# Performance work log

Hardware: AMD Instinct MI355X
Metric: run time of the kernel (lower is better)

The kernel has to match this reference:

```python
import jax, jax.numpy as jnp
import numpy as np

N, E = 100000, 1000000
IN_F, HID, OUT, K = 64, 64, 32, 3


def setup_inputs() -> dict:
    key = jax.random.key(0)
    ks = jax.random.split(key, 8)
    s = 0.05
    return {
        "features": jax.random.normal(ks[0], (N, IN_F), dtype=jnp.float32),
        "src": jax.random.randint(ks[1], (E,), 0, N),
        "dst": jax.random.randint(ks[2], (E,), 0, N),
        "n_nodes": N,
        "W1": jax.random.normal(ks[3], (K * IN_F, HID), jnp.float32) * s,
        "b1": jnp.zeros((HID,), jnp.float32),
        "W2": jax.random.normal(ks[4], (K * HID, HID), jnp.float32) * s,
        "b2": jnp.zeros((HID,), jnp.float32),
        "Wm1": jax.random.normal(ks[5], (HID, HID), jnp.float32) * s,
        "bm1": jnp.zeros((HID,), jnp.float32),
        "Wm2": jax.random.normal(ks[6], (HID, OUT), jnp.float32) * s,
        "bm2": jnp.zeros((OUT,), jnp.float32),
    }


def _cheb_conv(x, src, dst, dinv, W, b, n_nodes, k=K):
    # DGL ChebConv with lambda_max = 2 (re_norm = 2/lambda_max = 1).
    def prop(h):  # D^{-1/2} A D^{-1/2} h via edge gather/scatter
        m = (h * dinv)[src]                                   # [E, F]
        agg = jax.ops.segment_sum(m, dst, num_segments=n_nodes)
        return agg * dinv

    X0 = x
    Xs = [X0]
    X1 = -prop(X0)                 # -re_norm*L h + (re_norm-1)*X0, re_norm=1
    Xs.append(X1)
    for _ in range(2, k):
        Xi = -2.0 * prop(X1) - X0  # Chebyshev recursion
        Xs.append(Xi)
        X0, X1 = X1, Xi
    return jnp.concatenate(Xs, axis=1) @ W + b  # Linear(k*F_in -> F_out)


def reference(features, src, dst, n_nodes, W1, b1, W2, b2, Wm1, bm1, Wm2, bm2):
    deg = jax.ops.segment_sum(
        jnp.ones((src.shape[0],), dtype=features.dtype), dst, num_segments=n_nodes
    )
    dinv = (jnp.clip(deg, 1.0, None) ** -0.5)[:, None]  # in-degree^{-1/2}
    x = jax.nn.relu(_cheb_conv(features, src, dst, dinv, W1, b1, n_nodes))
    x = jax.nn.relu(_cheb_conv(x, src, dst, dinv, W2, b2, n_nodes))
    return jax.nn.relu(x @ Wm1 + bm1) @ Wm2 + bm2
```

## Files before the change

kernel.cpp:

```cpp
#include <hip/hip_runtime.h>


typedef unsigned short ushort_t;
typedef __attribute__((ext_vector_type(8))) short v8s;
typedef __attribute__((ext_vector_type(4))) float v4f;

__device__ inline ushort_t f2bf(float f) {
    unsigned u = __float_as_uint(f);
    return (ushort_t)((u + 0x7FFFu + ((u >> 16) & 1u)) >> 16);
}
__device__ inline float bf2f(ushort_t h) {
    return __uint_as_float(((unsigned)h) << 16);
}

#define BSH 9
#define BSZ (1 << BSH)
#define CHUNK 4096

__global__ void k_wprep(const float* __restrict__ W1, const float* __restrict__ W2,
                        const float* __restrict__ Wm1, const float* __restrict__ Wm2,
                        ushort_t* __restrict__ W1t, ushort_t* __restrict__ W2t,
                        ushort_t* __restrict__ Wm1t, ushort_t* __restrict__ Wm2t,
                        int* __restrict__ gbase, int NB) {
    int i = blockIdx.x * 256 + threadIdx.x;
    if (i < 12288) { int k = i >> 6, n = i & 63; W1t[n * 192 + k] = f2bf(W1[i]); return; }
    i -= 12288;
    if (i < 12288) { int k = i >> 6, n = i & 63; W2t[n * 192 + k] = f2bf(W2[i]); return; }
    i -= 12288;
    if (i < 4096) { int k = i >> 6, n = i & 63; Wm1t[n * 64 + k] = f2bf(Wm1[i]); return; }
    i -= 4096;
    if (i < 2048) { int k = i >> 5, n = i & 31; Wm2t[n * 64 + k] = f2bf(Wm2[i]); return; }
    i -= 2048;
    if (i < NB) gbase[i] = 0;
}


__global__ __launch_bounds__(256) void k_bhist(const int* __restrict__ dst,
                                               int* __restrict__ gbase, int E, int NB) {
    __shared__ int h[1024];
    for (int i = threadIdx.x; i < NB; i += 256) h[i] = 0;
    __syncthreads();
    for (int i = blockIdx.x * blockDim.x + threadIdx.x; i < E; i += gridDim.x * blockDim.x)
        atomicAdd(&h[dst[i] >> BSH], 1);
    __syncthreads();
    for (int i = threadIdx.x; i < NB; i += 256)
        if (h[i]) atomicAdd(&gbase[i], h[i]);
}

__global__ void k_bscan(int* __restrict__ gbase, int* __restrict__ gcur, int NB) {
    __shared__ int sh[1024];
    int t = threadIdx.x;
    int v = (t < NB) ? gbase[t] : 0;
    sh[t] = v;
    __syncthreads();
    for (int off = 1; off < 1024; off <<= 1) {
        int u = 0;
        if (t >= off) u = sh[t - off];
        __syncthreads();
        sh[t] += u;
        __syncthreads();
    }
    if (t < NB) {
        int excl = sh[t] - v;
        gbase[t] = excl;
        gcur[t] = excl;
    }
}

__global__ __launch_bounds__(256) void k_bucket2(
    const int* __restrict__ src, const int* __restrict__ dst,
    int* __restrict__ gcur, int2* __restrict__ eb, int E, int NB) {
    __shared__ int ls[CHUNK];
    __shared__ int ld[CHUNK];
    __shared__ int hist[1024];
    __shared__ int bbase[1024];
    int t = threadIdx.x;
    int base = blockIdx.x * CHUNK;
    int count = E - base;
    if (count > CHUNK) count = CHUNK;
    for (int i = t; i < NB; i += 256) hist[i] = 0;
    __syncthreads();
    for (int i = t; i < count; i += 256) {
        int s = src[base + i];
        int d = dst[base + i];
        ls[i] = s;
        ld[i] = d;
        atomicAdd(&hist[d >> BSH], 1);
    }
    __syncthreads();
    for (int b = t; b < NB; b += 256) {
        int c = hist[b];
        bbase[b] = c ? atomicAdd(&gcur[b], c) : 0;
        hist[b] = 0;
    }
    __syncthreads();
    for (int i = t; i < count; i += 256) {
        int d = ld[i];
        int b = d >> BSH;
        int off = atomicAdd(&hist[b], 1);
        eb[bbase[b] + off] = make_int2(ls[i], d);
    }
}

__global__ __launch_bounds__(256) void k_local(
    const int2* __restrict__ eb, const int* __restrict__ gbase,
    int* __restrict__ col, int* __restrict__ row_ptr,
    float* __restrict__ dinv, int N, int E, int NB) {
    __shared__ int cnt[BSZ];
    __shared__ int tsum[256];
    int t = threadIdx.x;
    int b = blockIdx.x;
    int d0 = b << BSH;
    cnt[2 * t] = 0;
    cnt[2 * t + 1] = 0;
    __syncthreads();
    int beg = gbase[b];
    int end = (b + 1 < NB) ? gbase[b + 1] : E;
    for (int i = beg + t; i < end; i += 256)
        atomicAdd(&cnt[eb[i].y - d0], 1);
    __syncthreads();
    int c0 = cnt[2 * t], c1 = cnt[2 * t + 1];
    int mysum = c0 + c1;
    tsum[t] = mysum;
    __syncthreads();
    for (int off = 1; off < 256; off <<= 1) {
        int u = 0;
        if (t >= off) u = tsum[t - off];
        __syncthreads();
        tsum[t] += u;
        __syncthreads();
    }
    int rbase = beg + tsum[t] - mysum;
    int d = d0 + 2 * t;
    if (d < N) {
        row_ptr[d] = rbase;
        dinv[d] = rsqrtf(fmaxf((float)c0, 1.0f));
    }
    if (d + 1 < N) {
        row_ptr[d + 1] = rbase + c0;
        dinv[d + 1] = rsqrtf(fmaxf((float)c1, 1.0f));
    }
    cnt[2 * t] = rbase;
    cnt[2 * t + 1] = rbase + c0;
    __syncthreads();
    for (int i = beg + t; i < end; i += 256) {
        int2 e = eb[i];
        int p = atomicAdd(&cnt[e.y - d0], 1);
        col[p] = e.x;
    }
    if (b == NB - 1 && t == 0) row_ptr[N] = E;
}

__global__ void k_tobf16(const float4* __restrict__ X, const float* __restrict__ dinv,
                         ushort4* __restrict__ Y, int n4) {
    int i = blockIdx.x * blockDim.x + threadIdx.x;
    if (i < n4) {
        float s = dinv[i >> 4];
        float4 v = X[i];
        ushort4 o;
        o.x = f2bf(v.x * s); o.y = f2bf(v.y * s); o.z = f2bf(v.z * s); o.w = f2bf(v.w * s);
        Y[i] = o;
    }
}

template <int MODE>
__global__ __launch_bounds__(256) void k_prop(
    const ushort_t* __restrict__ Xb, const int* __restrict__ rp,
    const int* __restrict__ col, const float* __restrict__ dinv,
    const ushort_t* __restrict__ X0b, ushort_t* __restrict__ OUTB, int N) {
    int wid = (blockIdx.x * blockDim.x + threadIdx.x) >> 6;
    int lane = threadIdx.x & 63;
    if (wid >= N) return;
    int g = lane >> 4;
    int fl = (lane & 15) * 4;
    int beg = rp[wid], end = rp[wid + 1];
    float4 a0 = make_float4(0.f, 0.f, 0.f, 0.f);
    float4 a1 = make_float4(0.f, 0.f, 0.f, 0.f);
    int e = beg + g;
    for (; e + 4 < end; e += 8) {
        int s0 = col[e], s1 = col[e + 4];
        ushort4 u0 = *(const ushort4*)&Xb[(size_t)s0 * 64 + fl];
        ushort4 u1 = *(const ushort4*)&Xb[(size_t)s1 * 64 + fl];
        a0.x += bf2f(u0.x); a0.y += bf2f(u0.y); a0.z += bf2f(u0.z); a0.w += bf2f(u0.w);
        a1.x += bf2f(u1.x); a1.y += bf2f(u1.y); a1.z += bf2f(u1.z); a1.w += bf2f(u1.w);
    }
    if (e < end) {
        int s0 = col[e];
        ushort4 u0 = *(const ushort4*)&Xb[(size_t)s0 * 64 + fl];
        a0.x += bf2f(u0.x); a0.y += bf2f(u0.y); a0.z += bf2f(u0.z); a0.w += bf2f(u0.w);
    }
    float4 acc;
    acc.x = a0.x + a1.x;
    acc.y = a0.y + a1.y;
    acc.z = a0.z + a1.z;
    acc.w = a0.w + a1.w;
    acc.x += __shfl_xor(acc.x, 16);
    acc.y += __shfl_xor(acc.y, 16);
    acc.z += __shfl_xor(acc.z, 16);
    acc.w += __shfl_xor(acc.w, 16);
    acc.x += __shfl_xor(acc.x, 32);
    acc.y += __shfl_xor(acc.y, 32);
    acc.z += __shfl_xor(acc.z, 32);
    acc.w += __shfl_xor(acc.w, 32);
    if (g == 0) {
        float di = dinv[wid];
        ushort4 ob;
        if (MODE == 1) {
            float m = -di * di;
            ob.x = f2bf(m * acc.x);
            ob.y = f2bf(m * acc.y);
            ob.z = f2bf(m * acc.z);
            ob.w = f2bf(m * acc.w);
        } else {
            ushort4 x0u = *(const ushort4*)&X0b[(size_t)wid * 64 + fl];
            float m = -2.0f * di;
            float rd = 1.0f / di;
            ob.x = f2bf(fmaf(m, acc.x, -rd * bf2f(x0u.x)));
            ob.y = f2bf(fmaf(m, acc.y, -rd * bf2f(x0u.y)));
            ob.z = f2bf(fmaf(m, acc.z, -rd * bf2f(x0u.z)));
            ob.w = f2bf(fmaf(m, acc.w, -rd * bf2f(x0u.w)));
        }
        *(ushort4*)&OUTB[(size_t)wid * 64 + fl] = ob;
    }
}

template <bool SCALE_OUT>
__global__ __launch_bounds__(256) void k_cheb_mfma(
    const ushort_t* __restrict__ X0, const ushort_t* __restrict__ X1,
    const ushort_t* __restrict__ X2, const float* __restrict__ dinv,
    const ushort_t* __restrict__ Wt, const float* __restrict__ b,
    ushort_t* __restrict__ Yb, int N) {
    int wave = threadIdx.x >> 6, lane = threadIdx.x & 63;
    int n16 = lane & 15, q = lane >> 4;
    int node0 = blockIdx.x * 64;
    int arow = node0 + wave * 16 + n16;
    const ushort_t* Xc[3] = {X0, X1, X2};

    v4f acc_s[4], acc_u[4];
#pragma unroll
    for (int t = 0; t < 4; t++) {
        acc_s[t] = (v4f){0.f, 0.f, 0.f, 0.f};
        acc_u[t] = (v4f){0.f, 0.f, 0.f, 0.f};
    }
#pragma unroll
    for (int ks = 0; ks < 6; ks++) {
        int c = ks >> 1;
        int kk = (ks & 1) * 32 + q * 8;
        v8s av = {0, 0, 0, 0, 0, 0, 0, 0};
        if (arow < N) av = *(const v8s*)&Xc[c][(size_t)arow * 64 + kk];
#pragma unroll
        for (int t = 0; t < 4; t++) {
            v8s bv = *(const v8s*)&Wt[(size_t)(t * 16 + n16) * 192 + ks * 32 + q * 8];
            if (c < 2)
                acc_s[t] = __builtin_amdgcn_mfma_f32_16x16x32_bf16(av, bv, acc_s[t], 0, 0, 0);
            else
                acc_u[t] = __builtin_amdgcn_mfma_f32_16x16x32_bf16(av, bv, acc_u[t], 0, 0, 0);
        }
    }
    int rbase = node0 + wave * 16 + q * 4;
#pragma unroll
    for (int r = 0; r < 4; r++) {
        int row = rbase + r;
        if (row < N) {
            float dv = dinv[row];
            float rd = 1.0f / dv;
            float s = SCALE_OUT ? dv : 1.0f;
#pragma unroll
            for (int t = 0; t < 4; t++) {
                float y = fmaf(rd, acc_s[t][r], acc_u[t][r]) + b[t * 16 + n16];
                y = fmaxf(y, 0.0f);
                Yb[(size_t)row * 64 + t * 16 + n16] = f2bf(s * y);
            }
        }
    }
}

__global__ __launch_bounds__(256) void k_mlp_mfma(
    const ushort_t* __restrict__ Hb, const ushort_t* __restrict__ W1t,
    const float* __restrict__ b1, const ushort_t* __restrict__ W2t,
    const float* __restrict__ b2, float* __restrict__ out, int N) {
    __shared__ ushort_t Hs[64][76];
    int wave = threadIdx.x >> 6, lane = threadIdx.x & 63;
    int n16 = lane & 15, q = lane >> 4;
    int node0 = blockIdx.x * 64;
    int arow = node0 + wave * 16 + n16;

    v4f acc[4];
#pragma unroll
    for (int t = 0; t < 4; t++) acc[t] = (v4f){0.f, 0.f, 0.f, 0.f};
#pragma unroll
    for (int ks = 0; ks < 2; ks++) {
        v8s av = {0, 0, 0, 0, 0, 0, 0, 0};
        if (arow < N) av = *(const v8s*)&Hb[(size_t)arow * 64 + ks * 32 + q * 8];
#pragma unroll
        for (int t = 0; t < 4; t++) {
            v8s bv = *(const v8s*)&W1t[(size_t)(t * 16 + n16) * 64 + ks * 32 + q * 8];
            acc[t] = __builtin_amdgcn_mfma_f32_16x16x32_bf16(av, bv, acc[t], 0, 0, 0);
        }
    }
    int lr = wave * 16 + q * 4;
#pragma unroll
    for (int r = 0; r < 4; r++)
#pragma unroll
        for (int t = 0; t < 4; t++) {
            float y = acc[t][r] + b1[t * 16 + n16];
            Hs[lr + r][t * 16 + n16] = f2bf(fmaxf(y, 0.0f));
        }
    __syncthreads();

    v4f a2[2];
    a2[0] = (v4f){0.f, 0.f, 0.f, 0.f};
    a2[1] = (v4f){0.f, 0.f, 0.f, 0.f};
#pragma unroll
    for (int ks = 0; ks < 2; ks++) {
        v8s av = *(const v8s*)&Hs[wave * 16 + n16][ks * 32 + q * 8];
#pragma unroll
        for (int t = 0; t < 2; t++) {
            v8s bv = *(const v8s*)&W2t[(size_t)(t * 16 + n16) * 64 + ks * 32 + q * 8];
            a2[t] = __builtin_amdgcn_mfma_f32_16x16x32_bf16(av, bv, a2[t], 0, 0, 0);
        }
    }
    int rbase = node0 + wave * 16 + q * 4;
#pragma unroll
    for (int r = 0; r < 4; r++) {
        int row = rbase + r;
        if (row < N) {
#pragma unroll
            for (int t = 0; t < 2; t++)
                out[(size_t)row * 32 + t * 16 + n16] = a2[t][r] + b2[t * 16 + n16];
        }
    }
}

extern "C" void kernel_launch(void* const* d_in, const int* in_sizes, int n_in,
                              void* d_out, int out_size, void* d_ws, size_t ws_size,
                              hipStream_t stream) {
    const float* features = (const float*)d_in[0];
    const int* src = (const int*)d_in[1];
    const int* dst = (const int*)d_in[2];
    const float* W1 = (const float*)d_in[4];
    const float* b1 = (const float*)d_in[5];
    const float* W2 = (const float*)d_in[6];
    const float* b2 = (const float*)d_in[7];
    const float* Wm1 = (const float*)d_in[8];
    const float* bm1 = (const float*)d_in[9];
    const float* Wm2 = (const float*)d_in[10];
    const float* bm2 = (const float*)d_in[11];
    float* out = (float*)d_out;

    int N = in_sizes[0] / 64;
    int E = in_sizes[1];
    int NB = (N + BSZ - 1) >> BSH;

    float* ws = (float*)d_ws;
    float* dinv = ws;
    int* row_ptr = (int*)(dinv + N);
    int* gbase = row_ptr + (N + 1);
    int* gcur = gbase + 1024;
    int* col = gcur + 1024;
    int2* eb = (int2*)(((uintptr_t)(col + E) + 7) & ~(uintptr_t)7);
    ushort_t* Fb  = (ushort_t*)(eb + E);
    ushort_t* X1b = Fb  + (size_t)N * 64;
    ushort_t* X2b = X1b + (size_t)N * 64;
    ushort_t* H1b = X2b + (size_t)N * 64;
    ushort_t* H2b = H1b + (size_t)N * 64;
    ushort_t* W1t = H2b + (size_t)N * 64;
    ushort_t* W2t = W1t + 64 * 192;
    ushort_t* Wm1t = W2t + 64 * 192;
    ushort_t* Wm2t = Wm1t + 64 * 64;

    int pblk = (N * 64 + 255) / 256;
    int gblk = (N + 63) / 64;
    int n4 = N * 16;
    int cblk = (n4 + 255) / 256;
    int bblk = (E + CHUNK - 1) / CHUNK;

    k_wprep<<<(30720 + 1024 + 255) / 256, 256, 0, stream>>>(
        W1, W2, Wm1, Wm2, W1t, W2t, Wm1t, Wm2t, gbase, NB);

    k_bhist<<<512, 256, 0, stream>>>(dst, gbase, E, NB);
    k_bscan<<<1, 1024, 0, stream>>>(gbase, gcur, NB);
    k_bucket2<<<bblk, 256, 0, stream>>>(src, dst, gcur, eb, E, NB);
    k_local<<<NB, 256, 0, stream>>>(eb, gbase, col, row_ptr, dinv, N, E, NB);

    k_tobf16<<<cblk, 256, 0, stream>>>((const float4*)features, dinv, (ushort4*)Fb, n4);

    k_prop<1><<<pblk, 256, 0, stream>>>(Fb, row_ptr, col, dinv, nullptr, X1b, N);
    k_prop<2><<<pblk, 256, 0, stream>>>(X1b, row_ptr, col, dinv, Fb, X2b, N);
    k_cheb_mfma<true><<<gblk, 256, 0, stream>>>(Fb, X1b, X2b, dinv, W1t, b1, H1b, N);

    k_prop<1><<<pblk, 256, 0, stream>>>(H1b, row_ptr, col, dinv, nullptr, X1b, N);
    k_prop<2><<<pblk, 256, 0, stream>>>(X1b, row_ptr, col, dinv, H1b, X2b, N);
    k_cheb_mfma<false><<<gblk, 256, 0, stream>>>(H1b, X1b, X2b, dinv, W2t, b2, H2b, N);

    k_mlp_mfma<<<gblk, 256, 0, stream>>>(H2b, Wm1t, bm1, Wm2t, bm2, out, N);
}
```

Before: 388.6 us.

## Build CSR with global atomic counting sort and fuse second ChebConv with MLP

Replaces the two-level bucketed CSR build (bucket histogram, bucket scatter, per-bucket local sort) with per-node global atomic degree counting, a two-pass block scan, and a direct atomic scatter into col. It also fuses the second Chebyshev linear layer with the two-layer MLP head, keeping the hidden activations in shared memory instead of writing and rereading H2. The simpler CSR build drops the intermediate edge buffer and launches, but relies on contended global atomics with random access, and column order within a row becomes nondeterministic.

Result: slower. 452.8 us (+16.5%).

```diff
diff --git a/kernel.cpp b/kernel.cpp
--- a/kernel.cpp
+++ b/kernel.cpp
@@ -12,16 +12,12 @@
 __device__ inline float bf2f(ushort_t h) {
     return __uint_as_float(((unsigned)h) << 16);
 }
-
-#define BSH 9
-#define BSZ (1 << BSH)
-#define CHUNK 4096
 
 __global__ void k_wprep(const float* __restrict__ W1, const float* __restrict__ W2,
                         const float* __restrict__ Wm1, const float* __restrict__ Wm2,
                         ushort_t* __restrict__ W1t, ushort_t* __restrict__ W2t,
                         ushort_t* __restrict__ Wm1t, ushort_t* __restrict__ Wm2t,
-                        int* __restrict__ gbase, int NB) {
+                        int* __restrict__ deg, int N) {
     int i = blockIdx.x * 256 + threadIdx.x;
     if (i < 12288) { int k = i >> 6, n = i & 63; W1t[n * 192 + k] = f2bf(W1[i]); return; }
     i -= 12288;
@@ -31,124 +27,86 @@
     i -= 4096;
     if (i < 2048) { int k = i >> 5, n = i & 31; Wm2t[n * 64 + k] = f2bf(Wm2[i]); return; }
     i -= 2048;
-    if (i < NB) gbase[i] = 0;
-}
-
-
-__global__ __launch_bounds__(256) void k_bhist(const int* __restrict__ dst,
-                                               int* __restrict__ gbase, int E, int NB) {
-    __shared__ int h[1024];
-    for (int i = threadIdx.x; i < NB; i += 256) h[i] = 0;
-    __syncthreads();
-    for (int i = blockIdx.x * blockDim.x + threadIdx.x; i < E; i += gridDim.x * blockDim.x)
-        atomicAdd(&h[dst[i] >> BSH], 1);
-    __syncthreads();
-    for (int i = threadIdx.x; i < NB; i += 256)
-        if (h[i]) atomicAdd(&gbase[i], h[i]);
-}
-
-__global__ void k_bscan(int* __restrict__ gbase, int* __restrict__ gcur, int NB) {
+    if (i < N) deg[i] = 0;
+}
+
+
+__global__ __launch_bounds__(256) void k_deg(const int* __restrict__ dst,
+                                             int* __restrict__ deg, int E) {
+    int base = blockIdx.x * 1024 + threadIdx.x;
+#pragma unroll
+    for (int k = 0; k < 4; k++) {
+        int i = base + k * 256;
+        if (i < E) atomicAdd(&deg[dst[i]], 1);
+    }
+}
+
+__global__ __launch_bounds__(1024) void k_scanA(const int* __restrict__ deg,
+                                                int* __restrict__ row_ptr,
+                                                int* __restrict__ psum,
+                                                float* __restrict__ dinv, int N) {
     __shared__ int sh[1024];
     int t = threadIdx.x;
-    int v = (t < NB) ? gbase[t] : 0;
+    int i = blockIdx.x * 1024 + t;
+    int v = (i < N) ? deg[i] : 0;
     sh[t] = v;
+    if (i < N) dinv[i] = rsqrtf(fmaxf((float)v, 1.0f));
     __syncthreads();
     for (int off = 1; off < 1024; off <<= 1) {
-        int u = 0;
-        if (t >= off) u = sh[t - off];
+        int u = (t >= off) ? sh[t - off] : 0;
         __syncthreads();
         sh[t] += u;
         __syncthreads();
     }
-    if (t < NB) {
-        int excl = sh[t] - v;
-        gbase[t] = excl;
-        gcur[t] = excl;
-    }
-}
-
-__global__ __launch_bounds__(256) void k_bucket2(
-    const int* __restrict__ src, const int* __restrict__ dst,
-    int* __restrict__ gcur, int2* __restrict__ eb, int E, int NB) {
-    __shared__ int ls[CHUNK];
-    __shared__ int ld[CHUNK];
-    __shared__ int hist[1024];
-    __shared__ int bbase[1024];
-    int t = threadIdx.x;
-    int base = blockIdx.x * CHUNK;
-    int count = E - base;
-    if (count > CHUNK) count = CHUNK;
-    for (int i = t; i < NB; i += 256) hist[i] = 0;
-    __syncthreads();
-    for (int i = t; i < count; i += 256) {
-        int s = src[base + i];
-        int d = dst[base + i];
-        ls[i] = s;
-        ld[i] = d;
-        atomicAdd(&hist[d >> BSH], 1);
-    }
-    __syncthreads();
-    for (int b = t; b < NB; b += 256) {
-        int c = hist[b];
-        bbase[b] = c ? atomicAdd(&gcur[b], c) : 0;
-        hist[b] = 0;
-    }
-    __syncthreads();
-    for (int i = t; i < count; i += 256) {
-        int d = ld[i];
-        int b = d >> BSH;
-        int off = atomicAdd(&hist[b], 1);
-        eb[bbase[b] + off] = make_int2(ls[i], d);
-    }
-}
-
-__global__ __launch_bounds__(256) void k_local(
-    const int2* __restrict__ eb, const int* __restrict__ gbase,
-    int* __restrict__ col, int* __restrict__ row_ptr,
-    float* __restrict__ dinv, int N, int E, int NB) {
-    __shared__ int cnt[BSZ];
-    __shared__ int tsum[256];
-    int t = threadIdx.x;
-    int b = blockIdx.x;
-    int d0 = b << BSH;
-    cnt[2 * t] = 0;
-    cnt[2 * t + 1] = 0;
-    __syncthreads();
-    int beg = gbase[b];
-    int end = (b + 1 < NB) ? gbase[b + 1] : E;
-    for (int i = beg + t; i < end; i += 256)
-        atomicAdd(&cnt[eb[i].y - d0], 1);
-    __syncthreads();
-    int c0 = cnt[2 * t], c1 = cnt[2 * t + 1];
-    int mysum = c0 + c1;
-    tsum[t] = mysum;
-    __syncthreads();
-    for (int off = 1; off < 256; off <<= 1) {
-        int u = 0;
-        if (t >= off) u = tsum[t - off];
-        __syncthreads();
-        tsum[t] += u;
-        __syncthreads();
-    }
-    int rbase = beg + tsum[t] - mysum;
-    int d = d0 + 2 * t;
-    if (d < N) {
-        row_ptr[d] = rbase;
-        dinv[d] = rsqrtf(fmaxf((float)c0, 1.0f));
-    }
-    if (d + 1 < N) {
-        row_ptr[d + 1] = rbase + c0;
-        dinv[d + 1] = rsqrtf(fmaxf((float)c1, 1.0f));
-    }
-    cnt[2 * t] = rbase;
-    cnt[2 * t + 1] = rbase + c0;
-    __syncthreads();
-    for (int i = beg + t; i < end; i += 256) {
-        int2 e = eb[i];
-        int p = atomicAdd(&cnt[e.y - d0], 1);
-        col[p] = e.x;
-    }
-    if (b == NB - 1 && t == 0) row_ptr[N] = E;
+    if (i < N) row_ptr[i] = sh[t] - v;
+    if (t == 1023) psum[blockIdx.x] = sh[1023];
+}
+
+__global__ __launch_bounds__(1024) void k_scanC(int* __restrict__ row_ptr,
+                                                int* __restrict__ gcur,
+                                                const int* __restrict__ psum,
+                                                int N, int E, int NBLK) {
+    __shared__ int red[17];
+    int t = threadIdx.x, b = blockIdx.x;
+    int v = (t < b) ? psum[t] : 0;
+    v += __shfl_down(v, 32);
+    v += __shfl_down(v, 16);
+    v += __shfl_down(v, 8);
+    v += __shfl_down(v, 4);
+    v += __shfl_down(v, 2);
+    v += __shfl_down(v, 1);
+    if ((t & 63) == 0) red[t >> 6] = v;
+    __syncthreads();
+    if (t == 0) {
+        int s = 0;
+        for (int w = 0; w < 16; w++) s += red[w];
+        red[16] = s;
+    }
+    __syncthreads();
+    int base = red[16];
+    int i = b * 1024 + t;
+    if (i < N) {
+        int r = row_ptr[i] + base;
+        row_ptr[i] = r;
+        gcur[i] = r;
+    }
+    if (b == NBLK - 1 && t == 0) row_ptr[N] = E;
+}
+
+__global__ __launch_bounds__(256) void k_scatter(const int* __restrict__ src,
+                                                 const int* __restrict__ dst,
+                                                 int* __restrict__ gcur,
+                                                 int* __restrict__ col, int E) {
+    int base = blockIdx.x * 1024 + threadIdx.x;
+#pragma unroll
+    for (int k = 0; k < 4; k++) {
+        int i = base + k * 256;
+        if (i < E) {
+            int s = src[i], d = dst[i];
+            int p = atomicAdd(&gcur[d], 1);
+            col[p] = s;
+        }
+    }
 }
 
 __global__ void k_tobf16(const float4* __restrict__ X, const float* __restrict__ dinv,
@@ -275,36 +233,80 @@
     }
 }
 
-__global__ __launch_bounds__(256) void k_mlp_mfma(
-    const ushort_t* __restrict__ Hb, const ushort_t* __restrict__ W1t,
-    const float* __restrict__ b1, const ushort_t* __restrict__ W2t,
-    const float* __restrict__ b2, float* __restrict__ out, int N) {
-    __shared__ ushort_t Hs[64][76];
+__global__ __launch_bounds__(256) void k_cheb_mlp(
+    const ushort_t* __restrict__ X0, const ushort_t* __restrict__ X1,
+    const ushort_t* __restrict__ X2, const float* __restrict__ dinv,
+    const ushort_t* __restrict__ Wt, const float* __restrict__ b,
+    const ushort_t* __restrict__ Wm1t, const float* __restrict__ bm1,
+    const ushort_t* __restrict__ Wm2t, const float* __restrict__ bm2,
+    float* __restrict__ out, int N) {
+    __shared__ ushort_t Hs0[64][76];
+    __shared__ ushort_t Hs1[64][76];
     int wave = threadIdx.x >> 6, lane = threadIdx.x & 63;
     int n16 = lane & 15, q = lane >> 4;
     int node0 = blockIdx.x * 64;
     int arow = node0 + wave * 16 + n16;
+    const ushort_t* Xc[3] = {X0, X1, X2};
+
+    v4f acc_s[4], acc_u[4];
+#pragma unroll
+    for (int t = 0; t < 4; t++) {
+        acc_s[t] = (v4f){0.f, 0.f, 0.f, 0.f};
+        acc_u[t] = (v4f){0.f, 0.f, 0.f, 0.f};
+    }
+#pragma unroll
+    for (int ks = 0; ks < 6; ks++) {
+        int c = ks >> 1;
+        int kk = (ks & 1) * 32 + q * 8;
+        v8s av = {0, 0, 0, 0, 0, 0, 0, 0};
+        if (arow < N) av = *(const v8s*)&Xc[c][(size_t)arow * 64 + kk];
+#pragma unroll
+        for (int t = 0; t < 4; t++) {
+            v8s bv = *(const v8s*)&Wt[(size_t)(t * 16 + n16) * 192 + ks * 32 + q * 8];
+            if (c < 2)
+                acc_s[t] = __builtin_amdgcn_mfma_f32_16x16x32_bf16(av, bv, acc_s[t], 0, 0, 0);
+            else
+                acc_u[t] = __builtin_amdgcn_mfma_f32_16x16x32_bf16(av, bv, acc_u[t], 0, 0, 0);
+        }
+    }
+    int lr = wave * 16 + q * 4;
+    int rbase = node0 + lr;
+#pragma unroll
+    for (int r = 0; r < 4; r++) {
+        int row = rbase + r;
+        if (row < N) {
+            float dv = dinv[row];
+            float rd = 1.0f / dv;
+#pragma unroll
+            for (int t = 0; t < 4; t++) {
+                float y = fmaf(rd, acc_s[t][r], acc_u[t][r]) + b[t * 16 + n16];
+                Hs0[lr + r][t * 16 + n16] = f2bf(fmaxf(y, 0.0f));
+            }
+        } else {
+#pragma unroll
+            for (int t = 0; t < 4; t++) Hs0[lr + r][t * 16 + n16] = 0;
+        }
+    }
+    __syncthreads();
 
     v4f acc[4];
 #pragma unroll
     for (int t = 0; t < 4; t++) acc[t] = (v4f){0.f, 0.f, 0.f, 0.f};
 #pragma unroll
     for (int ks = 0; ks < 2; ks++) {
-        v8s av = {0, 0, 0, 0, 0, 0, 0, 0};
-        if (arow < N) av = *(const v8s*)&Hb[(size_t)arow * 64 + ks * 32 + q * 8];
+        v8s av = *(const v8s*)&Hs0[wave * 16 + n16][ks * 32 + q * 8];
 #pragma unroll
         for (int t = 0; t < 4; t++) {
-            v8s bv = *(const v8s*)&W1t[(size_t)(t * 16 + n16) * 64 + ks * 32 + q * 8];
+            v8s bv = *(const v8s*)&Wm1t[(size_t)(t * 16 + n16) * 64 + ks * 32 + q * 8];
             acc[t] = __builtin_amdgcn_mfma_f32_16x16x32_bf16(av, bv, acc[t], 0, 0, 0);
         }
     }
-    int lr = wave * 16 + q * 4;
 #pragma unroll
     for (int r = 0; r < 4; r++)
 #pragma unroll
         for (int t = 0; t < 4; t++) {
-            float y = acc[t][r] + b1[t * 16 + n16];
-            Hs[lr + r][t * 16 + n16] = f2bf(fmaxf(y, 0.0f));
+            float y = acc[t][r] + bm1[t * 16 + n16];
+            Hs1[lr + r][t * 16 + n16] = f2bf(fmaxf(y, 0.0f));
         }
     __syncthreads();
 
@@ -313,21 +315,20 @@
     a2[1] = (v4f){0.f, 0.f, 0.f, 0.f};
 #pragma unroll
     for (int ks = 0; ks < 2; ks++) {
-        v8s av = *(const v8s*)&Hs[wave * 16 + n16][ks * 32 + q * 8];
+        v8s av = *(const v8s*)&Hs1[wave * 16 + n16][ks * 32 + q * 8];
 #pragma unroll
         for (int t = 0; t < 2; t++) {
-            v8s bv = *(const v8s*)&W2t[(size_t)(t * 16 + n16) * 64 + ks * 32 + q * 8];
+            v8s bv = *(const v8s*)&Wm2t[(size_t)(t * 16 + n16) * 64 + ks * 32 + q * 8];
             a2[t] = __builtin_amdgcn_mfma_f32_16x16x32_bf16(av, bv, a2[t], 0, 0, 0);
         }
     }
-    int rbase = node0 + wave * 16 + q * 4;
 #pragma unroll
     for (int r = 0; r < 4; r++) {
         int row = rbase + r;
         if (row < N) {
 #pragma unroll
             for (int t = 0; t < 2; t++)
-                out[(size_t)row * 32 + t * 16 + n16] = a2[t][r] + b2[t * 16 + n16];
+                out[(size_t)row * 32 + t * 16 + n16] = a2[t][r] + bm2[t * 16 + n16];
         }
     }
 }
@@ -350,21 +351,20 @@
 
     int N = in_sizes[0] / 64;
     int E = in_sizes[1];
-    int NB = (N + BSZ - 1) >> BSH;
+    int NBLK = (N + 1023) >> 10;
 
     float* ws = (float*)d_ws;
     float* dinv = ws;
     int* row_ptr = (int*)(dinv + N);
-    int* gbase = row_ptr + (N + 1);
-    int* gcur = gbase + 1024;
-    int* col = gcur + 1024;
-    int2* eb = (int2*)(((uintptr_t)(col + E) + 7) & ~(uintptr_t)7);
-    ushort_t* Fb  = (ushort_t*)(eb + E);
-    ushort_t* X1b = Fb  + (size_t)N * 64;
+    int* deg = row_ptr + (N + 1);
+    int* gcur = deg + N;
+    int* psum = gcur + N;
+    int* col = psum + 1024;
+    ushort_t* Fb = (ushort_t*)(((uintptr_t)(col + E) + 15) & ~(uintptr_t)15);
+    ushort_t* X1b = Fb + (size_t)N * 64;
     ushort_t* X2b = X1b + (size_t)N * 64;
     ushort_t* H1b = X2b + (size_t)N * 64;
-    ushort_t* H2b = H1b + (size_t)N * 64;
-    ushort_t* W1t = H2b + (size_t)N * 64;
+    ushort_t* W1t = H1b + (size_t)N * 64;
     ushort_t* W2t = W1t + 64 * 192;
     ushort_t* Wm1t = W2t + 64 * 192;
     ushort_t* Wm2t = Wm1t + 64 * 64;
@@ -373,15 +373,15 @@
     int gblk = (N + 63) / 64;
     int n4 = N * 16;
     int cblk = (n4 + 255) / 256;
-    int bblk = (E + CHUNK - 1) / CHUNK;
-
-    k_wprep<<<(30720 + 1024 + 255) / 256, 256, 0, stream>>>(
-        W1, W2, Wm1, Wm2, W1t, W2t, Wm1t, Wm2t, gbase, NB);
-
-    k_bhist<<<512, 256, 0, stream>>>(dst, gbase, E, NB);
-    k_bscan<<<1, 1024, 0, stream>>>(gbase, gcur, NB);
-    k_bucket2<<<bblk, 256, 0, stream>>>(src, dst, gcur, eb, E, NB);
-    k_local<<<NB, 256, 0, stream>>>(eb, gbase, col, row_ptr, dinv, N, E, NB);
+    int eblk = (E + 1023) / 1024;
+
+    k_wprep<<<(30720 + N + 255) / 256, 256, 0, stream>>>(
+        W1, W2, Wm1, Wm2, W1t, W2t, Wm1t, Wm2t, deg, N);
+
+    k_deg<<<eblk, 256, 0, stream>>>(dst, deg, E);
+    k_scanA<<<NBLK, 1024, 0, stream>>>(deg, row_ptr, psum, dinv, N);
+    k_scanC<<<NBLK, 1024, 0, stream>>>(row_ptr, gcur, psum, N, E, NBLK);
+    k_scatter<<<eblk, 256, 0, stream>>>(src, dst, gcur, col, E);
 
     k_tobf16<<<cblk, 256, 0, stream>>>((const float4*)features, dinv, (ushort4*)Fb, n4);
 
@@ -391,7 +391,6 @@
 
     k_prop<1><<<pblk, 256, 0, stream>>>(H1b, row_ptr, col, dinv, nullptr, X1b, N);
     k_prop<2><<<pblk, 256, 0, stream>>>(X1b, row_ptr, col, dinv, H1b, X2b, N);
-    k_cheb_mfma<false><<<gblk, 256, 0, stream>>>(H1b, X1b, X2b, dinv, W2t, b2, H2b, N);
-
-    k_mlp_mfma<<<gblk, 256, 0, stream>>>(H2b, Wm1t, bm1, Wm2t, bm2, out, N);
-}
+    k_cheb_mlp<<<gblk, 256, 0, stream>>>(H1b, X1b, X2b, dinv, W2t, b2,
+                                         Wm1t, bm1, Wm2t, bm2, out, N);
+}
```
